# Kernel tuning notes

Measured on AMD Instinct MI355X. Metric: run time of the kernel, lower is better.

## Reference

```python
import jax, jax.numpy as jnp
from jax import lax
import numpy as np

N_ITERS = 1000
LR = 0.1
EPS = 1e-8


def _log_mag_loss(sos, target_dB):
    """MSE between 20*log10(|sosfreqz(sos)|) and target_dB (matches LogMagTargetFrequencyLoss)."""
    n = target_dB.shape[-1]
    w = jnp.linspace(0.0, np.pi, n)            # [n] freqs in [0, pi]
    z1 = jnp.exp(-1j * w.astype(jnp.complex64))  # e^{-jw}, [n]
    z2 = z1 * z1                               # e^{-2jw}
    b = sos[:, :3].astype(jnp.complex64)       # [16,3] numerator coeffs
    a = sos[:, 3:].astype(jnp.complex64)       # [16,3] denominator coeffs
    # per-section response: (b0 + b1 z^-1 + b2 z^-2) / (a0 + a1 z^-1 + a2 z^-2), [16,n]
    B = b[:, 0:1] + b[:, 1:2] * z1[None, :] + b[:, 2:3] * z2[None, :]
    A = a[:, 0:1] + a[:, 1:2] * z1[None, :] + a[:, 2:3] * z2[None, :]
    H = jnp.prod(B / A, axis=0)                # cascade of sections, [n]
    mag = jnp.sqrt(jnp.real(H) ** 2 + jnp.imag(H) ** 2)
    input_dB = 20.0 * jnp.log10(mag + EPS)
    return jnp.mean((input_dB - target_dB) ** 2)


def setup_inputs() -> dict:
    key = jax.random.key(0)
    k1, k2 = jax.random.split(key)
    sos_init = jax.random.uniform(k1, (16, 6), dtype=jnp.float32)  # torch.rand(16,6)
    target_dB = jax.random.normal(k2, (512,), dtype=jnp.float32) * 6.0  # dB-scale target curve
    return {"sos_init": sos_init, "target_dB": target_dB}


def reference(sos_init, target_dB):
    grad_fn = jax.grad(_log_mag_loss)

    def step(sos, _):
        g = grad_fn(sos, target_dB)
        return sos - LR * g, None  # plain SGD step (no momentum)

    sos_final, _ = lax.scan(step, sos_init, None, length=N_ITERS)
    return sos_final
```

## Files before the change

### kernel.cpp

```cpp
#include <hip/hip_runtime.h>
#include <math.h>

#define TPB 1024

typedef float v2f __attribute__((ext_vector_type(2)));

static __device__ __forceinline__ v2f mk2(float x, float y) {
    v2f r; r.x = x; r.y = y; return r;
}
static __device__ __forceinline__ v2f fma2(v2f a, v2f b, v2f c) {
    return __builtin_elementwise_fma(a, b, c);
}
static __device__ __forceinline__ float rcp_nr(float x) {
    float r = __builtin_amdgcn_rcpf(x);
    return r * fmaf(-x, r, 2.0f);
}
static __device__ __forceinline__ v2f rcp2(v2f x) {
    v2f r;
    r.x = __builtin_amdgcn_rcpf(x.x);
    r.y = __builtin_amdgcn_rcpf(x.y);
    return r;
}

static __device__ __forceinline__ void quad_allsum2(float& a, float& b) {
    asm("s_nop 1\n\t"
        "v_add_f32 %0, %0, %0 quad_perm:[1,0,3,2] row_mask:0xf bank_mask:0xf bound_ctrl:0\n\t"
        "v_add_f32 %1, %1, %1 quad_perm:[1,0,3,2] row_mask:0xf bank_mask:0xf bound_ctrl:0\n\t"
        "s_nop 0\n\t"
        "v_add_f32 %0, %0, %0 quad_perm:[2,3,0,1] row_mask:0xf bank_mask:0xf bound_ctrl:0\n\t"
        "v_add_f32 %1, %1, %1 quad_perm:[2,3,0,1] row_mask:0xf bank_mask:0xf bound_ctrl:0"
        : "+v"(a), "+v"(b));
}

__device__ __forceinline__ void red6_s48(float i0, float i1, float i2,
                                         float i3, float i4, float i5,
                                         float& o0, float& o1, float& o2,
                                         float& o3, float& o4, float& o5) {
    asm("s_nop 1\n\t"
        "v_add_f32 %0, %6, %6  row_shr:4 row_mask:0xf bank_mask:0xf bound_ctrl:0\n\t"
        "v_add_f32 %3, %9, %9  row_shr:4 row_mask:0xf bank_mask:0xf bound_ctrl:0\n\t"
        "v_add_f32 %1, %7, %7  row_shr:4 row_mask:0xf bank_mask:0xf bound_ctrl:0\n\t"
        "v_add_f32 %4, %10, %10 row_shr:4 row_mask:0xf bank_mask:0xf bound_ctrl:0\n\t"
        "v_add_f32 %2, %8, %8  row_shr:4 row_mask:0xf bank_mask:0xf bound_ctrl:0\n\t"
        "v_add_f32 %5, %11, %11 row_shr:4 row_mask:0xf bank_mask:0xf bound_ctrl:0\n\t"
        "v_add_f32 %0, %0, %0 row_shr:8 row_mask:0xf bank_mask:0xf bound_ctrl:0\n\t"
        "v_add_f32 %3, %3, %3 row_shr:8 row_mask:0xf bank_mask:0xf bound_ctrl:0\n\t"
        "v_add_f32 %1, %1, %1 row_shr:8 row_mask:0xf bank_mask:0xf bound_ctrl:0\n\t"
        "v_add_f32 %4, %4, %4 row_shr:8 row_mask:0xf bank_mask:0xf bound_ctrl:0\n\t"
        "v_add_f32 %2, %2, %2 row_shr:8 row_mask:0xf bank_mask:0xf bound_ctrl:0\n\t"
        "v_add_f32 %5, %5, %5 row_shr:8 row_mask:0xf bank_mask:0xf bound_ctrl:0"
        : "=&v"(o0), "=&v"(o1), "=&v"(o2), "=&v"(o3), "=&v"(o4), "=&v"(o5)
        : "v"(i0), "v"(i1), "v"(i2), "v"(i3), "v"(i4), "v"(i5));
}

__device__ __forceinline__ float red1_g8(float g) {
    asm("s_nop 1\n\t"
        "v_add_f32 %0, %0, %0 row_shr:1 row_mask:0xf bank_mask:0xf bound_ctrl:0\n\t"
        "s_nop 1\n\t"
        "v_add_f32 %0, %0, %0 row_shr:2 row_mask:0xf bank_mask:0xf bound_ctrl:0\n\t"
        "s_nop 1\n\t"
        "v_add_f32 %0, %0, %0 row_shr:4 row_mask:0xf bank_mask:0xf bound_ctrl:0"
        : "+v"(g));
    return g;
}

__device__ __forceinline__ int cmap(int k) {
    return (k < 3) ? 2 * k : 2 * k - 5;
}

#define GPAD 100

__global__
__attribute__((amdgpu_flat_work_group_size(TPB, TPB), amdgpu_waves_per_eu(4, 4)))
void sgd_filter(const float* __restrict__ sos_in,
                const float* __restrict__ target,
                float* __restrict__ out) {
    __shared__ __align__(16) float sos[96];
    __shared__ __align__(16) float gpart[64][GPAD];

    const int tid = threadIdx.x;
    const int qd  = tid >> 2;
    const int pos = tid & 3;
    const float* secbase = &sos[pos * 24];

    if (tid < 96) sos[(tid / 6) * 6 + cmap(tid % 6)] = sos_in[tid];

    const int u    = tid >> 3;
    const int oct  = tid & 7;
    const int usec = u / 6, uk = u % 6;
    const int uscol = usec * 6 + cmap(uk);
    const bool upd = (tid < 768);
    const bool writer = upd && (oct == 7);
    float myc = 0.0f;
    if (writer) myc = sos_in[u];
    const float* urp = &gpart[oct][0] + u;

    const double step = 3.14159265358979323846 / 511.0;
    const float w0 = (float)((double)(2 * qd) * step);
    const float w1 = (float)((double)(2 * qd + 1) * step);
    const float c10 = cosf(w0), s10 = -sinf(w0);
    const float c20 = c10 * c10 - s10 * s10, s20 = 2.0f * c10 * s10;
    const float c11 = cosf(w1), s11 = -sinf(w1);
    const float c21 = c11 * c11 - s11 * s11, s21 = 2.0f * c11 * s11;
    const float2 tg = *(const float2*)&target[2 * qd];
    const float KC = 40.0f / (512.0f * 2.302585092994046f);

    const v2f c1v0 = mk2(c10, c10), s1v0 = mk2(s10, s10);
    const v2f c2v0 = mk2(c20, c20), s2v0 = mk2(s20, s20);
    const v2f c1v1 = mk2(c11, c11), s1v1 = mk2(s11, s11);
    const v2f c2v1 = mk2(c21, c21), s2v1 = mk2(s21, s21);

    __syncthreads();

    v2f RA0, RA1, RA2, RA3, IA0, IA1, IA2, IA3, VA0, VA1, VA2, VA3;
    v2f RB0, RB1, RB2, RB3, IB0, IB1, IB2, IB3, VB0, VB1, VB2, VB3;

#define SEC_EVAL(sl, BA0, BA1, BA2)                                          \
    {                                                                        \
        const v2f ba0 = BA0, ba1 = BA1, ba2 = BA2;                           \
        RA##sl = fma2(ba2, c2v0, fma2(ba1, c1v0, ba0));                      \
        IA##sl = fma2(ba2, s2v0, ba1 * s1v0);                                \
        {                                                                    \
            const v2f n = fma2(RA##sl, RA##sl, IA##sl * IA##sl);             \
            prod0 = prod0 * n;                                               \
            VA##sl = rcp2(n);                                                \
        }                                                                    \
        RB##sl = fma2(ba2, c2v1, fma2(ba1, c1v1, ba0));                      \
        IB##sl = fma2(ba2, s2v1, ba1 * s1v1);                                \
        {                                                                    \
            const v2f n = fma2(RB##sl, RB##sl, IB##sl * IB##sl);             \
            prod1 = prod1 * n;                                               \
            VB##sl = rcp2(n);                                                \
        }                                                                    \
    }

#define SEC_BWD(sl)                                                          \
    {                                                                        \
        const v2f KA = KK0 * VA##sl;                                         \
        const v2f PA = KA * RA##sl;                                          \
        const v2f QA = KA * IA##sl;                                          \
        const v2f KB = KK1 * VB##sl;                                         \
        const v2f PB = KB * RB##sl;                                          \
        const v2f QB = KB * IB##sl;                                          \
        const v2f P  = PA + PB;                                              \
        const v2f G1 = fma2(c1v0, PA, s1v0 * QA) + fma2(c1v1, PB, s1v1 * QB);\
        const v2f G2 = fma2(c2v0, PA, s2v0 * QA) + fma2(c2v1, PB, s2v1 * QB);\
        float g0, g1, g2, g3, g4, g5;                                        \
        red6_s48(P.x, G1.x, G2.x, P.y, G1.y, G2.y,                           \
                 g0, g1, g2, g3, g4, g5);                                    \
        if ((tid & 15) >= 12) {                                              \
            float* p = &gpart[tid >> 4][24 * pos + 6 * (sl)];                \
            *(float4*)p       = make_float4(g0, g1, g2, g3);                 \
            *(float2*)(p + 4) = make_float2(g4, g5);                         \
        }                                                                    \
    }

    for (int it = 0; it < 1000; ++it) {
        const float4 q0 = *(const float4*)(secbase + 0);
        const float4 q1 = *(const float4*)(secbase + 4);
        const float4 q2 = *(const float4*)(secbase + 8);
        const float4 q3 = *(const float4*)(secbase + 12);
        const float4 q4 = *(const float4*)(secbase + 16);
        const float4 q5 = *(const float4*)(secbase + 20);
        v2f prod0 = mk2(1.0f, 1.0f), prod1 = mk2(1.0f, 1.0f);
        SEC_EVAL(0, mk2(q0.x, q0.y), mk2(q0.z, q0.w), mk2(q1.x, q1.y))
        SEC_EVAL(1, mk2(q1.z, q1.w), mk2(q2.x, q2.y), mk2(q2.z, q2.w))
        SEC_EVAL(2, mk2(q3.x, q3.y), mk2(q3.z, q3.w), mk2(q4.x, q4.y))
        SEC_EVAL(3, mk2(q4.z, q4.w), mk2(q5.x, q5.y), mk2(q5.z, q5.w))
        float L0 = __builtin_amdgcn_logf(prod0.x) - __builtin_amdgcn_logf(prod0.y);
        float L1 = __builtin_amdgcn_logf(prod1.x) - __builtin_amdgcn_logf(prod1.y);

        quad_allsum2(L0, L1);

        const float mag0   = __builtin_amdgcn_exp2f(0.5f * L0);
        const float magpe0 = mag0 + 1e-8f;
        const float indB0  = 6.020599913279624f * __builtin_amdgcn_logf(magpe0);
        const float K0 = KC * (indB0 - tg.x) * mag0 * rcp_nr(magpe0);
        const float mag1   = __builtin_amdgcn_exp2f(0.5f * L1);
        const float magpe1 = mag1 + 1e-8f;
        const float indB1  = 6.020599913279624f * __builtin_amdgcn_logf(magpe1);
        const float K1 = KC * (indB1 - tg.y) * mag1 * rcp_nr(magpe1);
        const v2f KK0 = mk2(K0, -K0);
        const v2f KK1 = mk2(K1, -K1);

        SEC_BWD(0) SEC_BWD(1) SEC_BWD(2) SEC_BWD(3)
        __syncthreads();

        if (upd) {
            const float r0 = urp[0],        r1 = urp[1 * 8 * GPAD];
            const float r2 = urp[2 * 8 * GPAD], r3 = urp[3 * 8 * GPAD];
            const float r4 = urp[4 * 8 * GPAD], r5 = urp[5 * 8 * GPAD];
            const float r6 = urp[6 * 8 * GPAD], r7 = urp[7 * 8 * GPAD];
            float g = red1_g8(((r0 + r1) + (r2 + r3)) + ((r4 + r5) + (r6 + r7)));
            if (writer) {
                myc = fmaf(-0.1f, g, myc);
                sos[uscol] = myc;
            }
        }
        __syncthreads();
    }

    if (writer) out[u] = myc;
}

extern "C" void kernel_launch(void* const* d_in, const int* in_sizes, int n_in,
                              void* d_out, int out_size, void* d_ws, size_t ws_size,
                              hipStream_t stream) {
    const float* sos_in = (const float*)d_in[0];
    const float* target = (const float*)d_in[1];
    float* outp = (float*)d_out;
    hipLaunchKernelGGL(sgd_filter, dim3(1), dim3(TPB), 0, stream, sos_in, target, outp);
}
```

Before: 2.213 ms.

## Batch section reciprocals, drop Newton step, shorten DPP reduction into larger LDS

Per-section reciprocals of |A|^2-like terms are now computed from a single reciprocal of the product of four norms, using prefix products, instead of four separate rcp calls per frequency. The Newton refinement on the loss-scale reciprocal is dropped. The in-wave gradient reduction now stops after the row_shr:8 step, writing twice as many partials into a doubled LDS buffer, and the update threads sum 16 partials instead of 8. This trades transcendental and DPP work for extra LDS traffic and slightly lower precision, with a possible overflow or underflow risk in the product of norms.

After: 2.014 ms. 1.1x faster.

```diff
diff --git a/kernel.cpp b/kernel.cpp
--- a/kernel.cpp
+++ b/kernel.cpp
@@ -10,10 +10,6 @@
 }
 static __device__ __forceinline__ v2f fma2(v2f a, v2f b, v2f c) {
     return __builtin_elementwise_fma(a, b, c);
-}
-static __device__ __forceinline__ float rcp_nr(float x) {
-    float r = __builtin_amdgcn_rcpf(x);
-    return r * fmaf(-x, r, 2.0f);
 }
 static __device__ __forceinline__ v2f rcp2(v2f x) {
     v2f r;
@@ -32,23 +28,17 @@
         : "+v"(a), "+v"(b));
 }
 
-__device__ __forceinline__ void red6_s48(float i0, float i1, float i2,
-                                         float i3, float i4, float i5,
-                                         float& o0, float& o1, float& o2,
-                                         float& o3, float& o4, float& o5) {
+__device__ __forceinline__ void red6_s8(float i0, float i1, float i2,
+                                        float i3, float i4, float i5,
+                                        float& o0, float& o1, float& o2,
+                                        float& o3, float& o4, float& o5) {
     asm("s_nop 1\n\t"
-        "v_add_f32 %0, %6, %6  row_shr:4 row_mask:0xf bank_mask:0xf bound_ctrl:0\n\t"
-        "v_add_f32 %3, %9, %9  row_shr:4 row_mask:0xf bank_mask:0xf bound_ctrl:0\n\t"
-        "v_add_f32 %1, %7, %7  row_shr:4 row_mask:0xf bank_mask:0xf bound_ctrl:0\n\t"
-        "v_add_f32 %4, %10, %10 row_shr:4 row_mask:0xf bank_mask:0xf bound_ctrl:0\n\t"
-        "v_add_f32 %2, %8, %8  row_shr:4 row_mask:0xf bank_mask:0xf bound_ctrl:0\n\t"
-        "v_add_f32 %5, %11, %11 row_shr:4 row_mask:0xf bank_mask:0xf bound_ctrl:0\n\t"
-        "v_add_f32 %0, %0, %0 row_shr:8 row_mask:0xf bank_mask:0xf bound_ctrl:0\n\t"
-        "v_add_f32 %3, %3, %3 row_shr:8 row_mask:0xf bank_mask:0xf bound_ctrl:0\n\t"
-        "v_add_f32 %1, %1, %1 row_shr:8 row_mask:0xf bank_mask:0xf bound_ctrl:0\n\t"
-        "v_add_f32 %4, %4, %4 row_shr:8 row_mask:0xf bank_mask:0xf bound_ctrl:0\n\t"
-        "v_add_f32 %2, %2, %2 row_shr:8 row_mask:0xf bank_mask:0xf bound_ctrl:0\n\t"
-        "v_add_f32 %5, %5, %5 row_shr:8 row_mask:0xf bank_mask:0xf bound_ctrl:0"
+        "v_add_f32 %0, %6, %6  row_shr:8 row_mask:0xf bank_mask:0xf bound_ctrl:0\n\t"
+        "v_add_f32 %3, %9, %9  row_shr:8 row_mask:0xf bank_mask:0xf bound_ctrl:0\n\t"
+        "v_add_f32 %1, %7, %7  row_shr:8 row_mask:0xf bank_mask:0xf bound_ctrl:0\n\t"
+        "v_add_f32 %4, %10, %10 row_shr:8 row_mask:0xf bank_mask:0xf bound_ctrl:0\n\t"
+        "v_add_f32 %2, %8, %8  row_shr:8 row_mask:0xf bank_mask:0xf bound_ctrl:0\n\t"
+        "v_add_f32 %5, %11, %11 row_shr:8 row_mask:0xf bank_mask:0xf bound_ctrl:0"
         : "=&v"(o0), "=&v"(o1), "=&v"(o2), "=&v"(o3), "=&v"(o4), "=&v"(o5)
         : "v"(i0), "v"(i1), "v"(i2), "v"(i3), "v"(i4), "v"(i5));
 }
@@ -76,7 +66,7 @@
                 const float* __restrict__ target,
                 float* __restrict__ out) {
     __shared__ __align__(16) float sos[96];
-    __shared__ __align__(16) float gpart[64][GPAD];
+    __shared__ __align__(16) float gpart[128][GPAD];
 
     const int tid = threadIdx.x;
     const int qd  = tid >> 2;
@@ -114,45 +104,39 @@
 
     v2f RA0, RA1, RA2, RA3, IA0, IA1, IA2, IA3, VA0, VA1, VA2, VA3;
     v2f RB0, RB1, RB2, RB3, IB0, IB1, IB2, IB3, VB0, VB1, VB2, VB3;
-
-#define SEC_EVAL(sl, BA0, BA1, BA2)                                          \
-    {                                                                        \
-        const v2f ba0 = BA0, ba1 = BA1, ba2 = BA2;                           \
-        RA##sl = fma2(ba2, c2v0, fma2(ba1, c1v0, ba0));                      \
-        IA##sl = fma2(ba2, s2v0, ba1 * s1v0);                                \
-        {                                                                    \
-            const v2f n = fma2(RA##sl, RA##sl, IA##sl * IA##sl);             \
-            prod0 = prod0 * n;                                               \
-            VA##sl = rcp2(n);                                                \
-        }                                                                    \
-        RB##sl = fma2(ba2, c2v1, fma2(ba1, c1v1, ba0));                      \
-        IB##sl = fma2(ba2, s2v1, ba1 * s1v1);                                \
-        {                                                                    \
-            const v2f n = fma2(RB##sl, RB##sl, IB##sl * IB##sl);             \
-            prod1 = prod1 * n;                                               \
-            VB##sl = rcp2(n);                                                \
-        }                                                                    \
+    v2f NA0, NA1, NA2, NA3, NB0, NB1, NB2, NB3;
+
+#define SEC_EVAL(sl, BA0, BA1, BA2)                                         \
+    {                                                                       \
+        const v2f ba0 = BA0, ba1 = BA1, ba2 = BA2;                          \
+        RA##sl = fma2(ba2, c2v0, fma2(ba1, c1v0, ba0));                     \
+        IA##sl = fma2(ba2, s2v0, ba1 * s1v0);                               \
+        NA##sl = fma2(RA##sl, RA##sl, IA##sl * IA##sl);                     \
+        RB##sl = fma2(ba2, c2v1, fma2(ba1, c1v1, ba0));                     \
+        IB##sl = fma2(ba2, s2v1, ba1 * s1v1);                               \
+        NB##sl = fma2(RB##sl, RB##sl, IB##sl * IB##sl);                     \
     }
 
-#define SEC_BWD(sl)                                                          \
-    {                                                                        \
-        const v2f KA = KK0 * VA##sl;                                         \
-        const v2f PA = KA * RA##sl;                                          \
-        const v2f QA = KA * IA##sl;                                          \
-        const v2f KB = KK1 * VB##sl;                                         \
-        const v2f PB = KB * RB##sl;                                          \
-        const v2f QB = KB * IB##sl;                                          \
-        const v2f P  = PA + PB;                                              \
+#define SEC_BWD(sl)                                                         \
+    {                                                                       \
+        const v2f KA = KK0 * VA##sl;                                        \
+        const v2f PA = KA * RA##sl;                                         \
+        const v2f QA = KA * IA##sl;                                         \
+        const v2f KB = KK1 * VB##sl;                                        \
+        const v2f PB = KB * RB##sl;                                         \
+        const v2f QB = KB * IB##sl;                                         \
+        const v2f P  = PA + PB;                                             \
         const v2f G1 = fma2(c1v0, PA, s1v0 * QA) + fma2(c1v1, PB, s1v1 * QB);\
         const v2f G2 = fma2(c2v0, PA, s2v0 * QA) + fma2(c2v1, PB, s2v1 * QB);\
-        float g0, g1, g2, g3, g4, g5;                                        \
-        red6_s48(P.x, G1.x, G2.x, P.y, G1.y, G2.y,                           \
-                 g0, g1, g2, g3, g4, g5);                                    \
-        if ((tid & 15) >= 12) {                                              \
-            float* p = &gpart[tid >> 4][24 * pos + 6 * (sl)];                \
-            *(float4*)p       = make_float4(g0, g1, g2, g3);                 \
-            *(float2*)(p + 4) = make_float2(g4, g5);                         \
-        }                                                                    \
+        float g0, g1, g2, g3, g4, g5;                                       \
+        red6_s8(P.x, G1.x, G2.x, P.y, G1.y, G2.y,                           \
+                g0, g1, g2, g3, g4, g5);                                    \
+        if ((tid & 15) >= 8) {                                              \
+            float* p = &gpart[((tid >> 4) << 1) | ((tid >> 2) & 1)]         \
+                             [24 * pos + 6 * (sl)];                         \
+            *(float4*)p       = make_float4(g0, g1, g2, g3);                \
+            *(float2*)(p + 4) = make_float2(g4, g5);                        \
+        }                                                                   \
     }
 
     for (int it = 0; it < 1000; ++it) {
@@ -162,24 +146,37 @@
         const float4 q3 = *(const float4*)(secbase + 12);
         const float4 q4 = *(const float4*)(secbase + 16);
         const float4 q5 = *(const float4*)(secbase + 20);
-        v2f prod0 = mk2(1.0f, 1.0f), prod1 = mk2(1.0f, 1.0f);
         SEC_EVAL(0, mk2(q0.x, q0.y), mk2(q0.z, q0.w), mk2(q1.x, q1.y))
         SEC_EVAL(1, mk2(q1.z, q1.w), mk2(q2.x, q2.y), mk2(q2.z, q2.w))
         SEC_EVAL(2, mk2(q3.x, q3.y), mk2(q3.z, q3.w), mk2(q4.x, q4.y))
         SEC_EVAL(3, mk2(q4.z, q4.w), mk2(q5.x, q5.y), mk2(q5.z, q5.w))
-        float L0 = __builtin_amdgcn_logf(prod0.x) - __builtin_amdgcn_logf(prod0.y);
-        float L1 = __builtin_amdgcn_logf(prod1.x) - __builtin_amdgcn_logf(prod1.y);
+
+        const v2f tA01 = NA0 * NA1, tA23 = NA2 * NA3;
+        const v2f mA   = tA01 * tA23;
+        const v2f iA   = rcp2(mA);
+        const v2f iA01 = iA * tA23, iA23 = iA * tA01;
+        VA0 = iA01 * NA1; VA1 = iA01 * NA0;
+        VA2 = iA23 * NA3; VA3 = iA23 * NA2;
+        const v2f tB01 = NB0 * NB1, tB23 = NB2 * NB3;
+        const v2f mB   = tB01 * tB23;
+        const v2f iB   = rcp2(mB);
+        const v2f iB01 = iB * tB23, iB23 = iB * tB01;
+        VB0 = iB01 * NB1; VB1 = iB01 * NB0;
+        VB2 = iB23 * NB3; VB3 = iB23 * NB2;
+
+        float L0 = __builtin_amdgcn_logf(mA.x) - __builtin_amdgcn_logf(mA.y);
+        float L1 = __builtin_amdgcn_logf(mB.x) - __builtin_amdgcn_logf(mB.y);
 
         quad_allsum2(L0, L1);
 
         const float mag0   = __builtin_amdgcn_exp2f(0.5f * L0);
         const float magpe0 = mag0 + 1e-8f;
         const float indB0  = 6.020599913279624f * __builtin_amdgcn_logf(magpe0);
-        const float K0 = KC * (indB0 - tg.x) * mag0 * rcp_nr(magpe0);
+        const float K0 = KC * (indB0 - tg.x) * mag0 * __builtin_amdgcn_rcpf(magpe0);
         const float mag1   = __builtin_amdgcn_exp2f(0.5f * L1);
         const float magpe1 = mag1 + 1e-8f;
         const float indB1  = 6.020599913279624f * __builtin_amdgcn_logf(magpe1);
-        const float K1 = KC * (indB1 - tg.y) * mag1 * rcp_nr(magpe1);
+        const float K1 = KC * (indB1 - tg.y) * mag1 * __builtin_amdgcn_rcpf(magpe1);
         const v2f KK0 = mk2(K0, -K0);
         const v2f KK1 = mk2(K1, -K1);
 
@@ -187,11 +184,19 @@
         __syncthreads();
 
         if (upd) {
-            const float r0 = urp[0],        r1 = urp[1 * 8 * GPAD];
-            const float r2 = urp[2 * 8 * GPAD], r3 = urp[3 * 8 * GPAD];
-            const float r4 = urp[4 * 8 * GPAD], r5 = urp[5 * 8 * GPAD];
-            const float r6 = urp[6 * 8 * GPAD], r7 = urp[7 * 8 * GPAD];
-            float g = red1_g8(((r0 + r1) + (r2 + r3)) + ((r4 + r5) + (r6 + r7)));
+            const float r0  = urp[0],        r1  = urp[1 * 800];
+            const float r2  = urp[2 * 800],  r3  = urp[3 * 800];
+            const float r4  = urp[4 * 800],  r5  = urp[5 * 800];
+            const float r6  = urp[6 * 800],  r7  = urp[7 * 800];
+            const float r8  = urp[8 * 800],  r9  = urp[9 * 800];
+            const float r10 = urp[10 * 800], r11 = urp[11 * 800];
+            const float r12 = urp[12 * 800], r13 = urp[13 * 800];
+            const float r14 = urp[14 * 800], r15 = urp[15 * 800];
+            const float t0 = (r0 + r1) + (r2 + r3);
+            const float t1 = (r4 + r5) + (r6 + r7);
+            const float t2 = (r8 + r9) + (r10 + r11);
+            const float t3 = (r12 + r13) + (r14 + r15);
+            float g = red1_g8((t0 + t1) + (t2 + t3));
             if (writer) {
                 myc = fmaf(-0.1f, g, myc);
                 sos[uscol] = myc;
```
